# Kernel tuning notes

Measured on AMD Instinct MI355X. Metric: run time of the kernel, lower is better.

## Reference

```python
import jax, jax.numpy as jnp
import numpy as np

F_DIM = 1024
HEAD = 16
MLP_H = 4096
EPS = 1e-5


def _layernorm(x, g, b):
    mu = jnp.mean(x, axis=-1, keepdims=True)
    var = jnp.var(x, axis=-1, keepdims=True)
    return (x - mu) * jax.lax.rsqrt(var + EPS) * g + b


def setup_inputs() -> dict:
    key = jax.random.key(0)
    ks = jax.random.split(key, 16)
    B, T, F = 2, 2048, F_DIM
    s = 1.0 / np.sqrt(F)
    sm = 1.0 / np.sqrt(MLP_H)
    return {
        "x": jax.random.normal(ks[0], (B, T, F), jnp.float32),
        "ln1_g": jnp.ones((F,), jnp.float32),
        "ln1_b": jnp.zeros((F,), jnp.float32),
        "Wq": jax.random.normal(ks[1], (F, F), jnp.float32) * s,
        "bq": jnp.zeros((F,), jnp.float32),
        "Wk": jax.random.normal(ks[2], (F, F), jnp.float32) * s,
        "bk": jnp.zeros((F,), jnp.float32),
        "Wv": jax.random.normal(ks[3], (F, F), jnp.float32) * s,
        "bv": jnp.zeros((F,), jnp.float32),
        "Wo": jax.random.normal(ks[4], (F, F), jnp.float32) * s,
        "bo": jnp.zeros((F,), jnp.float32),
        "ln2_g": jnp.ones((F,), jnp.float32),
        "ln2_b": jnp.zeros((F,), jnp.float32),
        "W1": jax.random.normal(ks[5], (F, MLP_H), jnp.float32) * s,
        "b1": jnp.zeros((MLP_H,), jnp.float32),
        "W2": jax.random.normal(ks[6], (MLP_H, F), jnp.float32) * sm,
        "b2": jnp.zeros((F,), jnp.float32),
    }


def reference(x, ln1_g, ln1_b, Wq, bq, Wk, bk, Wv, bv, Wo, bo, ln2_g, ln2_b, W1, b1, W2, b2):
    B, T, F = x.shape
    H, Dh = HEAD, F // HEAD
    sqrt_d = jnp.asarray(F, x.dtype) ** 0.5  # NOTE: scale by sqrt(features), as in source

    h = _layernorm(x, ln1_g, ln1_b)
    Q = (h @ Wq + bq).reshape(B, T, H, Dh).transpose(0, 2, 1, 3)  # bhtd
    K = (h @ Wk + bk).reshape(B, T, H, Dh).transpose(0, 2, 1, 3)
    V = (h @ Wv + bv).reshape(B, T, H, Dh).transpose(0, 2, 1, 3)

    scores = jnp.einsum('bhif,bhjf->bhij', Q, K) / sqrt_d
    attn_map = jax.nn.softmax(scores, axis=-1)
    attn = jnp.einsum('bhij,bhjf->bihf', attn_map, V)  # [B,T,H,Dh]
    attn_out = attn.reshape(B, T, F) @ Wo + bo
    out = attn_out + x

    h2 = _layernorm(out, ln2_g, ln2_b)
    mlp = jax.nn.gelu(jax.nn.gelu(h2 @ W1 + b1, approximate=False) @ W2 + b2, approximate=False)
    return mlp + out
```

## Files before the change

### kernel.cpp

```cpp
#include <hip/hip_runtime.h>
#include <hip/hip_bf16.h>
#include <math.h>
#include <stdint.h>

typedef __attribute__((ext_vector_type(8))) __bf16 bf16x8;
typedef __attribute__((ext_vector_type(4))) float f32x4;

#define F_DIM 1024
#define MLP_HD 4096
#define HEADS 16
#define DH 64
#define B_SZ 2
#define T_SZ 2048
#define NROWS 4096
#define QKV_N 3072
#define LN_EPS 1e-5f

__device__ __forceinline__ void gload16(const void* g, void* l) {
    __builtin_amdgcn_global_load_lds(
        (const __attribute__((address_space(1))) uint32_t*)(uintptr_t)g,
        (__attribute__((address_space(3))) uint32_t*)(uintptr_t)l,
        16, 0, 0);
}

__global__ void transpose_cast(const float* __restrict__ in,
                               __hip_bfloat16* __restrict__ out,
                               int R, int C) {
    __shared__ float tile[32][33];
    int c0 = blockIdx.x * 32, r0 = blockIdx.y * 32;
    int tx = threadIdx.x, ty = threadIdx.y;
    #pragma unroll
    for (int i = 0; i < 32; i += 8)
        tile[ty + i][tx] = in[(size_t)(r0 + ty + i) * C + c0 + tx];
    __syncthreads();
    #pragma unroll
    for (int i = 0; i < 32; i += 8)
        out[(size_t)(c0 + ty + i) * R + r0 + tx] = __float2bfloat16(tile[tx][ty + i]);
}

__global__ void transpose_v(const __hip_bfloat16* __restrict__ QKV,
                            __hip_bfloat16* __restrict__ VT) {
    __shared__ __hip_bfloat16 tile[32][33];
    int dblk = blockIdx.y & 1, bh = blockIdx.y >> 1;
    int b = bh >> 4, h = bh & 15;
    int t0 = blockIdx.x * 32, d0 = dblk * 32;
    int tx = threadIdx.x, ty = threadIdx.y;
    #pragma unroll
    for (int i = 0; i < 32; i += 8)
        tile[ty + i][tx] = QKV[(size_t)(b * T_SZ + t0 + ty + i) * QKV_N + 2048 + h * DH + d0 + tx];
    __syncthreads();
    #pragma unroll
    for (int i = 0; i < 32; i += 8)
        VT[(size_t)(bh * DH + d0 + ty + i) * T_SZ + t0 + tx] = tile[tx][ty + i];
}

__global__ void concat_bias(const float* __restrict__ a, const float* __restrict__ b,
                            const float* __restrict__ c, float* __restrict__ o) {
    int i = blockIdx.x * 256 + threadIdx.x;
    o[i] = i < 1024 ? a[i] : (i < 2048 ? b[i - 1024] : c[i - 2048]);
}

__global__ void layernorm_bf16_k(const float* __restrict__ x,
                                 const float* __restrict__ g,
                                 const float* __restrict__ b,
                                 __hip_bfloat16* __restrict__ out) {
    int row = blockIdx.x;
    const float* xr = x + (size_t)row * F_DIM;
    int t = threadIdx.x;
    float4 v = ((const float4*)xr)[t];
    float s  = v.x + v.y + v.z + v.w;
    float s2 = v.x * v.x + v.y * v.y + v.z * v.z + v.w * v.w;
    #pragma unroll
    for (int off = 32; off >= 1; off >>= 1) {
        s  += __shfl_down(s, off);
        s2 += __shfl_down(s2, off);
    }
    __shared__ float rs_[4], rs2_[4];
    int wave = t >> 6, lane = t & 63;
    if (lane == 0) { rs_[wave] = s; rs2_[wave] = s2; }
    __syncthreads();
    float S  = rs_[0] + rs_[1] + rs_[2] + rs_[3];
    float S2 = rs2_[0] + rs2_[1] + rs2_[2] + rs2_[3];
    float mu  = S * (1.0f / F_DIM);
    float var = S2 * (1.0f / F_DIM) - mu * mu;
    float rstd = rsqrtf(var + LN_EPS);
    float4 gv = ((const float4*)g)[t];
    float4 bv = ((const float4*)b)[t];
    __hip_bfloat16* orow = out + (size_t)row * F_DIM;
    orow[t * 4 + 0] = __float2bfloat16((v.x - mu) * rstd * gv.x + bv.x);
    orow[t * 4 + 1] = __float2bfloat16((v.y - mu) * rstd * gv.y + bv.y);
    orow[t * 4 + 2] = __float2bfloat16((v.z - mu) * rstd * gv.z + bv.z);
    orow[t * 4 + 3] = __float2bfloat16((v.w - mu) * rstd * gv.w + bv.w);
}

__device__ __forceinline__ float gelu_exact(float x) {
    return 0.5f * x * (1.0f + erff(x * 0.70710678f));
}

#define MFMA_QUAD(AF, BF, MB, NB)                                              \
  do {                                                                         \
    __builtin_amdgcn_s_barrier();                                              \
    asm volatile("s_waitcnt lgkmcnt(0)" ::: "memory");                         \
    __builtin_amdgcn_sched_barrier(0);                                         \
    __builtin_amdgcn_s_setprio(1);                                             \
    _Pragma("unroll") for (int ks = 0; ks < 2; ++ks)                           \
      _Pragma("unroll") for (int a_ = 0; a_ < 4; ++a_)                         \
        _Pragma("unroll") for (int b_ = 0; b_ < 2; ++b_)                       \
          acc[(MB) + a_][(NB) + b_] = __builtin_amdgcn_mfma_f32_16x16x32_bf16( \
              AF[a_][ks], BF[b_][ks], acc[(MB) + a_][(NB) + b_], 0, 0, 0);     \
    __builtin_amdgcn_s_setprio(0);                                             \
  } while (0)

#define LDA_FRAGS(DST, BUF, MQ)                                                \
  do {                                                                         \
    _Pragma("unroll") for (int a_ = 0; a_ < 4; ++a_)                           \
      _Pragma("unroll") for (int ks = 0; ks < 2; ++ks) {                       \
        int row_ = (MQ) * 64 + a_ * 16 + fr;                                   \
        int byt_ = row_ * 128 + ((ks * 64 + fq * 16) ^ ((row_ & 7) << 4));     \
        DST[a_][ks] = *(const bf16x8*)((const char*)&LA[BUF][wm][0] + byt_);   \
      }                                                                        \
  } while (0)

#define LDB_FRAGS(DST, BUF, NQ)                                                \
  do {                                                                         \
    _Pragma("unroll") for (int b_ = 0; b_ < 2; ++b_)                           \
      _Pragma("unroll") for (int ks = 0; ks < 2; ++ks) {                       \
        int row_ = (wn & 1) * 64 + ((NQ) * 2 + b_) * 16 + fr;                  \
        int byt_ = row_ * 128 + ((ks * 64 + fq * 16) ^ ((row_ & 7) << 4));     \
        DST[b_][ks] = *(const bf16x8*)((const char*)&LB[BUF][hb][0] + byt_);   \
      }                                                                        \
  } while (0)

#define STAGE_A(BUF, H, KT_)                                                   \
  do {                                                                         \
    _Pragma("unroll") for (int q_ = 0; q_ < 2; ++q_)                           \
      gload16(A + (size_t)(m0 + (H) * 128 + srow[q_]) * K +                    \
                  (k00 + (KT_) * 64 + scol[q_]),                               \
              &LA[BUF][H][q_ * 4096 + t * 8]);                                 \
  } while (0)

#define STAGE_B(BUF, H, KT_)                                                   \
  do {                                                                         \
    _Pragma("unroll") for (int q_ = 0; q_ < 2; ++q_)                           \
      gload16(BT + (size_t)(n0 + (H) * 128 + srow[q_]) * K +                   \
                   (k00 + (KT_) * 64 + scol[q_]),                              \
              &LB[BUF][H][q_ * 4096 + t * 8]);                                 \
  } while (0)

template <int EPI>
__global__ __launch_bounds__(512, 2) void gemm256(
    const __hip_bfloat16* __restrict__ A,
    const __hip_bfloat16* __restrict__ BT,
    const float* __restrict__ bias,
    void* __restrict__ Cout,
    int M, int N, int K, int KLEN) {
    __shared__ __hip_bfloat16 LA[2][2][8192];
    __shared__ __hip_bfloat16 LB[2][2][8192];

    int t = threadIdx.x;
    int w = t >> 6, lane = t & 63;
    int wm = w >> 2, wn = w & 3;
    int fr = lane & 15, fq = lane >> 4;
    int hb = wn >> 1;
    int m0 = blockIdx.y * 256, n0 = blockIdx.x * 256;
    int k00 = blockIdx.z * KLEN;

    int srow[2], scol[2];
    #pragma unroll
    for (int q = 0; q < 2; ++q) {
        int u = q * 8192 + t * 16;
        u ^= ((u >> 7) & 7) << 4;
        srow[q] = u >> 7;
        scol[q] = (u & 127) >> 1;
    }

    f32x4 acc[8][4] = {};
    bf16x8 aflo[4][2], afhi[4][2], bflo[2][2], bfhi[2][2];
    int KT = KLEN >> 6;

    STAGE_A(0, 0, 0); STAGE_A(0, 1, 0); STAGE_B(0, 0, 0); STAGE_B(0, 1, 0);
    STAGE_A(1, 0, 1); STAGE_A(1, 1, 1);
    asm volatile("s_waitcnt vmcnt(4)" ::: "memory");
    __builtin_amdgcn_s_barrier();

    for (int i = 0;; ++i) {
        int k1 = 2 * i + 1;
        int nx2 = (2 * i + 2) % KT, nx3 = (2 * i + 3) % KT;
        LDA_FRAGS(aflo, 0, 0);
        LDB_FRAGS(bflo, 0, 0);
        STAGE_B(1, 0, k1);
        MFMA_QUAD(aflo, bflo, 0, 0);
        __builtin_amdgcn_s_barrier();
        LDA_FRAGS(afhi, 0, 1);
        STAGE_B(1, 1, k1);
        MFMA_QUAD(afhi, bflo, 4, 0);
        __builtin_amdgcn_s_barrier();
        LDB_FRAGS(bfhi, 0, 1);
        STAGE_A(0, 0, nx2);
        MFMA_QUAD(afhi, bfhi, 4, 2);
        __builtin_amdgcn_s_barrier();
        STAGE_A(0, 1, nx2);
        MFMA_QUAD(aflo, bfhi, 0, 2);
        asm volatile("s_waitcnt vmcnt(4)" ::: "memory");
        __builtin_amdgcn_s_barrier();
        LDA_FRAGS(aflo, 1, 0);
        LDB_FRAGS(bflo, 1, 0);
        STAGE_B(0, 0, nx2);
        MFMA_QUAD(aflo, bflo, 0, 0);
        __builtin_amdgcn_s_barrier();
        LDA_FRAGS(afhi, 1, 1);
        STAGE_B(0, 1, nx2);
        MFMA_QUAD(afhi, bflo, 4, 0);
        __builtin_amdgcn_s_barrier();
        LDB_FRAGS(bfhi, 1, 1);
        STAGE_A(1, 0, nx3);
        MFMA_QUAD(afhi, bfhi, 4, 2);
        __builtin_amdgcn_s_barrier();
        STAGE_A(1, 1, nx3);
        MFMA_QUAD(aflo, bfhi, 0, 2);
        asm volatile("s_waitcnt vmcnt(4)" ::: "memory");
        __builtin_amdgcn_s_barrier();
        if (2 * i + 2 >= KT) break;
    }

    #pragma unroll
    for (int ni = 0; ni < 4; ++ni) {
        int col = n0 + wn * 64 + ni * 16 + fr;
        float bv = (EPI == 4) ? 0.f : bias[col];
        #pragma unroll
        for (int mi = 0; mi < 8; ++mi) {
            #pragma unroll
            for (int j = 0; j < 4; ++j) {
                int row = m0 + wm * 128 + mi * 16 + fq * 4 + j;
                size_t idx = (size_t)row * N + col;
                float v = acc[mi][ni][j] + bv;
                if constexpr (EPI == 0) {
                    ((__hip_bfloat16*)Cout)[idx] = __float2bfloat16(v);
                } else if constexpr (EPI == 2) {
                    ((__hip_bfloat16*)Cout)[idx] = __float2bfloat16(gelu_exact(v));
                } else {
                    ((__hip_bfloat16*)Cout)[(size_t)blockIdx.z * ((size_t)M * N) + idx] =
                        __float2bfloat16(v);
                }
            }
        }
    }
}

__global__ __launch_bounds__(256) void mlp2_reduce(
    const __hip_bfloat16* __restrict__ P,
    const float* __restrict__ b2,
    const float* __restrict__ res,
    float* __restrict__ out) {
    int i = (blockIdx.x * 256 + threadIdx.x) * 8;
    float s[8] = {};
    #pragma unroll
    for (int sk = 0; sk < 4; ++sk) {
        bf16x8 v = *(const bf16x8*)&P[(size_t)sk * ((size_t)NROWS * F_DIM) + i];
        #pragma unroll
        for (int u = 0; u < 8; ++u) s[u] += (float)v[u];
    }
    int col = i & (F_DIM - 1);
    #pragma unroll
    for (int u = 0; u < 8; ++u)
        out[i + u] = gelu_exact(s[u] + b2[col + u]) + res[i + u];
}

template <int EPI, int BM>
__global__ __launch_bounds__(256) void gemm_bt(
    const __hip_bfloat16* __restrict__ A,
    const __hip_bfloat16* __restrict__ BT,
    const float* __restrict__ bias,
    const float* __restrict__ res,
    void* __restrict__ Cout,
    int M, int N, int K) {
    constexpr int MI = BM / 32;
    constexpr int AQ = BM / 64;
    __shared__ __hip_bfloat16 As[2][BM * 32];
    __shared__ __hip_bfloat16 Bs[2][128 * 32];

    int t = threadIdx.x;
    int m0 = blockIdx.y * BM, n0 = blockIdx.x * 128;
    int w = t >> 6, lane = t & 63;
    int wr = (w >> 1) * (BM / 2), wc = (w & 1) * 64;
    int fr = lane & 15, fq = lane >> 4;

    int scol = (lane & 3) * 8;
    int srowA = w * (BM / 4) + (lane >> 2);
    int srowB = w * 32 + (lane >> 2);
    const __hip_bfloat16* Ag = A  + (size_t)(m0 + srowA) * K + scol;
    const __hip_bfloat16* Bg = BT + (size_t)(n0 + srowB) * K + scol;
    int lofsA = w * (BM / 4) * 32 + lane * 8;
    int lofsB = w * 1024 + lane * 8;

    f32x4 acc[MI][4] = {};
    int KT = K >> 5;
    int cur = 0;

    #pragma unroll
    for (int q = 0; q < AQ; ++q)
        gload16(Ag + (size_t)q * 16 * K, &As[0][lofsA + q * 512]);
    #pragma unroll
    for (int q = 0; q < 2; ++q)
        gload16(Bg + (size_t)q * 16 * K, &Bs[0][lofsB + q * 512]);
    __syncthreads();

    for (int kt = 0; kt < KT; ++kt) {
        if (kt + 1 < KT) {
            const __hip_bfloat16* An = Ag + (size_t)(kt + 1) * 32;
            const __hip_bfloat16* Bn = Bg + (size_t)(kt + 1) * 32;
            #pragma unroll
            for (int q = 0; q < AQ; ++q)
                gload16(An + (size_t)q * 16 * K, &As[cur ^ 1][lofsA + q * 512]);
            #pragma unroll
            for (int q = 0; q < 2; ++q)
                gload16(Bn + (size_t)q * 16 * K, &Bs[cur ^ 1][lofsB + q * 512]);
        }
        bf16x8 af[MI], bfr[4];
        #pragma unroll
        for (int mi = 0; mi < MI; ++mi)
            af[mi] = *(const bf16x8*)&As[cur][(wr + mi * 16 + fr) * 32 + fq * 8];
        #pragma unroll
        for (int ni = 0; ni < 4; ++ni)
            bfr[ni] = *(const bf16x8*)&Bs[cur][(wc + ni * 16 + fr) * 32 + fq * 8];
        #pragma unroll
        for (int mi = 0; mi < MI; ++mi)
            #pragma unroll
            for (int ni = 0; ni < 4; ++ni)
                acc[mi][ni] = __builtin_amdgcn_mfma_f32_16x16x32_bf16(
                    af[mi], bfr[ni], acc[mi][ni], 0, 0, 0);
        __syncthreads();
        cur ^= 1;
    }

    #pragma unroll
    for (int ni = 0; ni < 4; ++ni) {
        int col = n0 + wc + ni * 16 + fr;
        float bv = bias[col];
        #pragma unroll
        for (int mi = 0; mi < MI; ++mi) {
            #pragma unroll
            for (int j = 0; j < 4; ++j) {
                int row = m0 + wr + mi * 16 + fq * 4 + j;
                size_t idx = (size_t)row * N + col;
                float v = acc[mi][ni][j] + bv;
                if constexpr (EPI == 1) {
                    ((float*)Cout)[idx] = v + res[idx];
                } else {
                    ((__hip_bfloat16*)Cout)[idx] = __float2bfloat16(v);
                }
            }
        }
    }
}

__global__ __launch_bounds__(256) void attn_mfma(
    const __hip_bfloat16* __restrict__ QKV,
    const __hip_bfloat16* __restrict__ VT,
    __hip_bfloat16* __restrict__ O) {
    __shared__ __hip_bfloat16 Kt[2][64][72];
    __shared__ __hip_bfloat16 Vt[2][64][72];
    __shared__ __hip_bfloat16 Ps[4][32][72];

    int blk = blockIdx.x;
    int qb = blk & 15;
    int bh = blk >> 4;
    int b = bh >> 4, h = bh & 15;
    int t = threadIdx.x;
    int w = t >> 6, lane = t & 63;
    int fr = lane & 15, fq = lane >> 4;

    bf16x8 qf[2][2];
    #pragma unroll
    for (int mt = 0; mt < 2; ++mt)
        #pragma unroll
        for (int ks = 0; ks < 2; ++ks) {
            int qrow = qb * 128 + w * 32 + mt * 16 + fr;
            const __hip_bfloat16* src =
                QKV + (size_t)(b * T_SZ + qrow) * QKV_N + h * DH + ks * 32 + fq * 8;
            bf16x8 v = *(const bf16x8*)src;
            #pragma unroll
            for (int u = 0; u < 8; ++u) v[u] = (__bf16)((float)v[u] * 0.03125f);
            qf[mt][ks] = v;
        }

    f32x4 oacc[2][4] = {};
    float lsum[2][4] = {};

    int sr = t >> 2;
    int sc = (t & 3) * 16;
    const __hip_bfloat16* Kg = QKV + (size_t)(b * T_SZ + sr) * QKV_N + F_DIM + h * DH + sc;
    const __hip_bfloat16* Vg = VT + (size_t)(bh * DH + sr) * T_SZ + sc;

    bf16x8 kr0, kr1, vr0, vr1;
    {
        kr0 = *(const bf16x8*)Kg;       kr1 = *(const bf16x8*)(Kg + 8);
        vr0 = *(const bf16x8*)Vg;       vr1 = *(const bf16x8*)(Vg + 8);
        *(bf16x8*)&Kt[0][sr][sc]     = kr0;
        *(bf16x8*)&Kt[0][sr][sc + 8] = kr1;
        *(bf16x8*)&Vt[0][sr][sc]     = vr0;
        *(bf16x8*)&Vt[0][sr][sc + 8] = vr1;
    }
    __syncthreads();

    int cur = 0;
    for (int j0 = 0; j0 < T_SZ; j0 += 64) {
        bool more = (j0 + 64 < T_SZ);
        if (more) {
            const __hip_bfloat16* kg = Kg + (size_t)(j0 + 64) * QKV_N;
            kr0 = *(const bf16x8*)kg;  kr1 = *(const bf16x8*)(kg + 8);
            const __hip_bfloat16* vg = Vg + (j0 + 64);
            vr0 = *(const bf16x8*)vg;  vr1 = *(const bf16x8*)(vg + 8);
        }

        f32x4 sacc[2][4] = {};
        __builtin_amdgcn_s_setprio(1);
        #pragma unroll
        for (int ks = 0; ks < 2; ++ks) {
            bf16x8 kf[4];
            #pragma unroll
            for (int nt = 0; nt < 4; ++nt)
                kf[nt] = *(const bf16x8*)&Kt[cur][nt * 16 + fr][ks * 32 + fq * 8];
            #pragma unroll
            for (int mt = 0; mt < 2; ++mt)
                #pragma unroll
                for (int nt = 0; nt < 4; ++nt)
                    sacc[mt][nt] = __builtin_amdgcn_mfma_f32_16x16x32_bf16(
                        qf[mt][ks], kf[nt], sacc[mt][nt], 0, 0, 0);
        }
        __builtin_amdgcn_s_setprio(0);

        #pragma unroll
        for (int mt = 0; mt < 2; ++mt) {
            #pragma unroll
            for (int r = 0; r < 4; ++r) {
                #pragma unroll
                for (int nt = 0; nt < 4; ++nt) {
                    float p = __expf(sacc[mt][nt][r]);
                    lsum[mt][r] += p;
                    Ps[w][mt * 16 + fq * 4 + r][nt * 16 + fr] = __float2bfloat16(p);
                }
            }
        }

        asm volatile("s_waitcnt lgkmcnt(0)" ::: "memory");
        __builtin_amdgcn_sched_barrier(0);

        __builtin_amdgcn_s_setprio(1);
        #pragma unroll
        for (int ks = 0; ks < 2; ++ks) {
            bf16x8 ap[2];
            #pragma unroll
            for (int mt = 0; mt < 2; ++mt)
                ap[mt] = *(const bf16x8*)&Ps[w][mt * 16 + fr][ks * 32 + fq * 8];
            #pragma unroll
            for (int nt = 0; nt < 4; ++nt) {
                bf16x8 vb = *(const bf16x8*)&Vt[cur][nt * 16 + fr][ks * 32 + fq * 8];
                #pragma unroll
                for (int mt = 0; mt < 2; ++mt)
                    oacc[mt][nt] = __builtin_amdgcn_mfma_f32_16x16x32_bf16(
                        ap[mt], vb, oacc[mt][nt], 0, 0, 0);
            }
        }
        __builtin_amdgcn_s_setprio(0);

        if (more) {
            *(bf16x8*)&Kt[cur ^ 1][sr][sc]     = kr0;
            *(bf16x8*)&Kt[cur ^ 1][sr][sc + 8] = kr1;
            *(bf16x8*)&Vt[cur ^ 1][sr][sc]     = vr0;
            *(bf16x8*)&Vt[cur ^ 1][sr][sc + 8] = vr1;
        }
        __syncthreads();
        cur ^= 1;
    }

    #pragma unroll
    for (int mt = 0; mt < 2; ++mt) {
        #pragma unroll
        for (int r = 0; r < 4; ++r) {
            float l = lsum[mt][r];
            #pragma unroll
            for (int d = 1; d < 16; d <<= 1) l += __shfl_xor(l, d);
            float rl = 1.0f / l;
            int row = qb * 128 + w * 32 + mt * 16 + fq * 4 + r;
            #pragma unroll
            for (int nt = 0; nt < 4; ++nt)
                O[(size_t)(b * T_SZ + row) * F_DIM + h * DH + nt * 16 + fr] =
                    __float2bfloat16(oacc[mt][nt][r] * rl);
        }
    }
}

extern "C" void kernel_launch(void* const* d_in, const int* in_sizes, int n_in,
                              void* d_out, int out_size, void* d_ws, size_t ws_size,
                              hipStream_t stream) {
    const float* x     = (const float*)d_in[0];
    const float* ln1_g = (const float*)d_in[1];
    const float* ln1_b = (const float*)d_in[2];
    const float* Wq    = (const float*)d_in[3];
    const float* bq    = (const float*)d_in[4];
    const float* Wk    = (const float*)d_in[5];
    const float* bk    = (const float*)d_in[6];
    const float* Wv    = (const float*)d_in[7];
    const float* bv    = (const float*)d_in[8];
    const float* Wo    = (const float*)d_in[9];
    const float* bo    = (const float*)d_in[10];
    const float* ln2_g = (const float*)d_in[11];
    const float* ln2_b = (const float*)d_in[12];
    const float* W1    = (const float*)d_in[13];
    const float* b1    = (const float*)d_in[14];
    const float* W2    = (const float*)d_in[15];
    const float* b2    = (const float*)d_in[16];
    float* outp = (float*)d_out;

    char* ws = (char*)d_ws;
    size_t off = 0;
    auto alloc = [&](size_t bytes) {
        void* p = ws + off;
        off += (bytes + 255) & ~(size_t)255;
        return p;
    };
    __hip_bfloat16* WqkvT = (__hip_bfloat16*)alloc((size_t)QKV_N * 1024 * 2);
    __hip_bfloat16* WoT   = (__hip_bfloat16*)alloc((size_t)1024 * 1024 * 2);
    __hip_bfloat16* W1T   = (__hip_bfloat16*)alloc((size_t)4096 * 1024 * 2);
    __hip_bfloat16* W2T   = (__hip_bfloat16*)alloc((size_t)4096 * 1024 * 2);
    float*          qkvb  = (float*)alloc((size_t)QKV_N * 4);
    __hip_bfloat16* h1    = (__hip_bfloat16*)alloc((size_t)NROWS * F_DIM * 2);
    __hip_bfloat16* QKVb  = (__hip_bfloat16*)alloc((size_t)NROWS * QKV_N * 2);
    __hip_bfloat16* VTb   = (__hip_bfloat16*)alloc((size_t)32 * DH * T_SZ * 2);
    __hip_bfloat16* attnO = (__hip_bfloat16*)alloc((size_t)NROWS * F_DIM * 2);
    float*          outb  = (float*)alloc((size_t)NROWS * F_DIM * 4);
    __hip_bfloat16* h2    = (__hip_bfloat16*)alloc((size_t)NROWS * F_DIM * 2);
    __hip_bfloat16* mlp1  = (__hip_bfloat16*)alloc((size_t)NROWS * MLP_HD * 2);
    __hip_bfloat16* mlp2P = h1;
    (void)ws_size; (void)in_sizes; (void)n_in; (void)out_size;

    dim3 tb(32, 8);
    transpose_cast<<<dim3(32, 32), tb, 0, stream>>>(Wq, WqkvT,               1024, 1024);
    transpose_cast<<<dim3(32, 32), tb, 0, stream>>>(Wk, WqkvT + 1024 * 1024, 1024, 1024);
    transpose_cast<<<dim3(32, 32), tb, 0, stream>>>(Wv, WqkvT + 2048 * 1024, 1024, 1024);
    transpose_cast<<<dim3(32, 32), tb, 0, stream>>>(Wo, WoT, 1024, 1024);
    transpose_cast<<<dim3(128, 32), tb, 0, stream>>>(W1, W1T, 1024, 4096);
    transpose_cast<<<dim3(32, 128), tb, 0, stream>>>(W2, W2T, 4096, 1024);
    concat_bias<<<12, 256, 0, stream>>>(bq, bk, bv, qkvb);

    layernorm_bf16_k<<<NROWS, 256, 0, stream>>>(x, ln1_g, ln1_b, h1);

    gemm256<0><<<dim3(QKV_N / 256, NROWS / 256, 1), 512, 0, stream>>>(
        h1, WqkvT, qkvb, QKVb, NROWS, QKV_N, 1024, 1024);

    transpose_v<<<dim3(T_SZ / 32, 64), tb, 0, stream>>>(QKVb, VTb);

    attn_mfma<<<512, 256, 0, stream>>>(QKVb, VTb, attnO);

    gemm_bt<1, 64><<<dim3(8, 64), 256, 0, stream>>>(attnO, WoT, bo, x, outb, NROWS, 1024, 1024);

    layernorm_bf16_k<<<NROWS, 256, 0, stream>>>(outb, ln2_g, ln2_b, h2);

    gemm256<2><<<dim3(MLP_HD / 256, NROWS / 256, 1), 512, 0, stream>>>(
        h2, W1T, b1, mlp1, NROWS, MLP_HD, 1024, 1024);

    gemm256<4><<<dim3(F_DIM / 256, NROWS / 256, 4), 512, 0, stream>>>(
        mlp1, W2T, nullptr, mlp2P, NROWS, F_DIM, MLP_HD, 1024);

    mlp2_reduce<<<2048, 256, 0, stream>>>(mlp2P, b2, outb, outp);
}
```

Before: 269.0 us.

## Stage GEMM epilogue through LDS, remap blocks per XCD, template KLEN

```diff
diff --git a/kernel.cpp b/kernel.cpp
--- a/kernel.cpp
+++ b/kernel.cpp
@@ -97,6 +97,9 @@
     return 0.5f * x * (1.0f + erff(x * 0.70710678f));
 }
 
+#define LA_PTR(BUF, H) ((__hip_bfloat16*)(SMEM + ((BUF) * 2 + (H)) * 16384))
+#define LB_PTR(BUF, H) ((__hip_bfloat16*)(SMEM + 65536 + ((BUF) * 2 + (H)) * 16384))
+
 #define MFMA_QUAD(AF, BF, MB, NB)                                              \
   do {                                                                         \
     __builtin_amdgcn_s_barrier();                                              \
@@ -117,7 +120,7 @@
       _Pragma("unroll") for (int ks = 0; ks < 2; ++ks) {                       \
         int row_ = (MQ) * 64 + a_ * 16 + fr;                                   \
         int byt_ = row_ * 128 + ((ks * 64 + fq * 16) ^ ((row_ & 7) << 4));     \
-        DST[a_][ks] = *(const bf16x8*)((const char*)&LA[BUF][wm][0] + byt_);   \
+        DST[a_][ks] = *(const bf16x8*)((const char*)LA_PTR(BUF, wm) + byt_);   \
       }                                                                        \
   } while (0)
 
@@ -127,7 +130,7 @@
       _Pragma("unroll") for (int ks = 0; ks < 2; ++ks) {                       \
         int row_ = (wn & 1) * 64 + ((NQ) * 2 + b_) * 16 + fr;                  \
         int byt_ = row_ * 128 + ((ks * 64 + fq * 16) ^ ((row_ & 7) << 4));     \
-        DST[b_][ks] = *(const bf16x8*)((const char*)&LB[BUF][hb][0] + byt_);   \
+        DST[b_][ks] = *(const bf16x8*)((const char*)LB_PTR(BUF, hb) + byt_);   \
       }                                                                        \
   } while (0)
 
@@ -136,7 +139,7 @@
     _Pragma("unroll") for (int q_ = 0; q_ < 2; ++q_)                           \
       gload16(A + (size_t)(m0 + (H) * 128 + srow[q_]) * K +                    \
                   (k00 + (KT_) * 64 + scol[q_]),                               \
-              &LA[BUF][H][q_ * 4096 + t * 8]);                                 \
+              LA_PTR(BUF, H) + q_ * 4096 + t * 8);                             \
   } while (0)
 
 #define STAGE_B(BUF, H, KT_)                                                   \
@@ -144,26 +147,37 @@
     _Pragma("unroll") for (int q_ = 0; q_ < 2; ++q_)                           \
       gload16(BT + (size_t)(n0 + (H) * 128 + srow[q_]) * K +                   \
                    (k00 + (KT_) * 64 + scol[q_]),                              \
-              &LB[BUF][H][q_ * 4096 + t * 8]);                                 \
+              LB_PTR(BUF, H) + q_ * 4096 + t * 8);                             \
   } while (0)
 
-template <int EPI>
+template <int EPI, int KLEN>
 __global__ __launch_bounds__(512, 2) void gemm256(
     const __hip_bfloat16* __restrict__ A,
     const __hip_bfloat16* __restrict__ BT,
     const float* __restrict__ bias,
     void* __restrict__ Cout,
-    int M, int N, int K, int KLEN) {
-    __shared__ __hip_bfloat16 LA[2][2][8192];
-    __shared__ __hip_bfloat16 LB[2][2][8192];
+    int M, int N, int K) {
+    __shared__ __align__(16) char SMEM[131072];
 
     int t = threadIdx.x;
     int w = t >> 6, lane = t & 63;
     int wm = w >> 2, wn = w & 3;
     int fr = lane & 15, fq = lane >> 4;
     int hb = wn >> 1;
-    int m0 = blockIdx.y * 256, n0 = blockIdx.x * 256;
-    int k00 = blockIdx.z * KLEN;
+
+    int gx = gridDim.x, gy = gridDim.y, gz = gridDim.z;
+    int bid = blockIdx.x + gx * (blockIdx.y + gy * blockIdx.z);
+    int nwg = gx * gy * gz;
+    int qch = nwg >> 3;
+    int logical = (bid & 7) * qch + (bid >> 3);
+    int pp = gy * gz;
+    int bx = logical / pp;
+    int rr = logical % pp;
+    int by = rr / gz;
+    int bz = rr % gz;
+
+    int m0 = by * 256, n0 = bx * 256;
+    int k00 = bz * KLEN;
 
     int srow[2], scol[2];
     #pragma unroll
@@ -176,7 +190,7 @@
 
     f32x4 acc[8][4] = {};
     bf16x8 aflo[4][2], afhi[4][2], bflo[2][2], bfhi[2][2];
-    int KT = KLEN >> 6;
+    constexpr int KT = KLEN >> 6;
 
     STAGE_A(0, 0, 0); STAGE_A(0, 1, 0); STAGE_B(0, 0, 0); STAGE_B(0, 1, 0);
     STAGE_A(1, 0, 1); STAGE_A(1, 1, 1);
@@ -185,7 +199,7 @@
 
     for (int i = 0;; ++i) {
         int k1 = 2 * i + 1;
-        int nx2 = (2 * i + 2) % KT, nx3 = (2 * i + 3) % KT;
+        int nx2 = (2 * i + 2) & (KT - 1), nx3 = (2 * i + 3) & (KT - 1);
         LDA_FRAGS(aflo, 0, 0);
         LDB_FRAGS(bflo, 0, 0);
         STAGE_B(1, 0, k1);
@@ -223,27 +237,36 @@
         if (2 * i + 2 >= KT) break;
     }
 
+    asm volatile("s_waitcnt vmcnt(0)" ::: "memory");
+    __builtin_amdgcn_s_barrier();
+
     #pragma unroll
     for (int ni = 0; ni < 4; ++ni) {
-        int col = n0 + wn * 64 + ni * 16 + fr;
-        float bv = (EPI == 4) ? 0.f : bias[col];
+        int col = wn * 64 + ni * 16 + fr;
+        float bv = (EPI == 4) ? 0.f : bias[n0 + col];
         #pragma unroll
         for (int mi = 0; mi < 8; ++mi) {
             #pragma unroll
             for (int j = 0; j < 4; ++j) {
-                int row = m0 + wm * 128 + mi * 16 + fq * 4 + j;
-                size_t idx = (size_t)row * N + col;
+                int row = wm * 128 + mi * 16 + fq * 4 + j;
                 float v = acc[mi][ni][j] + bv;
-                if constexpr (EPI == 0) {
-                    ((__hip_bfloat16*)Cout)[idx] = __float2bfloat16(v);
-                } else if constexpr (EPI == 2) {
-                    ((__hip_bfloat16*)Cout)[idx] = __float2bfloat16(gelu_exact(v));
-                } else {
-                    ((__hip_bfloat16*)Cout)[(size_t)blockIdx.z * ((size_t)M * N) + idx] =
-                        __float2bfloat16(v);
-                }
+                if constexpr (EPI == 2) v = gelu_exact(v);
+                int byt = row * 512 + ((col * 2) ^ ((row & 7) << 4));
+                *(__hip_bfloat16*)(SMEM + byt) = __float2bfloat16(v);
             }
         }
+    }
+    __builtin_amdgcn_s_barrier();
+
+    __hip_bfloat16* outc = (__hip_bfloat16*)Cout;
+    if constexpr (EPI == 4) outc += (size_t)bz * ((size_t)M * N);
+    #pragma unroll
+    for (int p = 0; p < 16; ++p) {
+        int row = p * 16 + (t >> 5);
+        int chunk = t & 31;
+        int byt = row * 512 + ((chunk * 16) ^ ((row & 7) << 4));
+        bf16x8 vv = *(const bf16x8*)(SMEM + byt);
+        *(bf16x8*)&outc[(size_t)(m0 + row) * N + n0 + chunk * 8] = vv;
     }
 }
 
@@ -430,6 +453,13 @@
         }
         __builtin_amdgcn_s_setprio(0);
 
+        bf16x8 vb[2][4];
+        #pragma unroll
+        for (int ks = 0; ks < 2; ++ks)
+            #pragma unroll
+            for (int nt = 0; nt < 4; ++nt)
+                vb[ks][nt] = *(const bf16x8*)&Vt[cur][nt * 16 + fr][ks * 32 + fq * 8];
+
         #pragma unroll
         for (int mt = 0; mt < 2; ++mt) {
             #pragma unroll
@@ -455,11 +485,10 @@
                 ap[mt] = *(const bf16x8*)&Ps[w][mt * 16 + fr][ks * 32 + fq * 8];
             #pragma unroll
             for (int nt = 0; nt < 4; ++nt) {
-                bf16x8 vb = *(const bf16x8*)&Vt[cur][nt * 16 + fr][ks * 32 + fq * 8];
                 #pragma unroll
                 for (int mt = 0; mt < 2; ++mt)
                     oacc[mt][nt] = __builtin_amdgcn_mfma_f32_16x16x32_bf16(
-                        ap[mt], vb, oacc[mt][nt], 0, 0, 0);
+                        ap[mt], vb[ks][nt], oacc[mt][nt], 0, 0, 0);
             }
         }
         __builtin_amdgcn_s_setprio(0);
@@ -546,8 +575,8 @@
 
     layernorm_bf16_k<<<NROWS, 256, 0, stream>>>(x, ln1_g, ln1_b, h1);
 
-    gemm256<0><<<dim3(QKV_N / 256, NROWS / 256, 1), 512, 0, stream>>>(
-        h1, WqkvT, qkvb, QKVb, NROWS, QKV_N, 1024, 1024);
+    gemm256<0, 1024><<<dim3(QKV_N / 256, NROWS / 256, 1), 512, 0, stream>>>(
+        h1, WqkvT, qkvb, QKVb, NROWS, QKV_N, 1024);
 
     transpose_v<<<dim3(T_SZ / 32, 64), tb, 0, stream>>>(QKVb, VTb);
 
@@ -557,11 +586,11 @@
 
     layernorm_bf16_k<<<NROWS, 256, 0, stream>>>(outb, ln2_g, ln2_b, h2);
 
-    gemm256<2><<<dim3(MLP_HD / 256, NROWS / 256, 1), 512, 0, stream>>>(
-        h2, W1T, b1, mlp1, NROWS, MLP_HD, 1024, 1024);
-
-    gemm256<4><<<dim3(F_DIM / 256, NROWS / 256, 4), 512, 0, stream>>>(
-        mlp1, W2T, nullptr, mlp2P, NROWS, F_DIM, MLP_HD, 1024);
+    gemm256<2, 1024><<<dim3(MLP_HD / 256, NROWS / 256, 1), 512, 0, stream>>>(
+        h2, W1T, b1, mlp1, NROWS, MLP_HD, 1024);
+
+    gemm256<4, 1024><<<dim3(F_DIM / 256, NROWS / 256, 4), 512, 0, stream>>>(
+        mlp1, W2T, nullptr, mlp2P, NROWS, F_DIM, MLP_HD);
 
     mlp2_reduce<<<2048, 256, 0, stream>>>(mlp2P, b2, outb, outp);
 }
```

After: 264.3 us. No clear change (-1.7%).
